# Kernel tuning notes

Measured on AMD Instinct MI355X. Metric: run time of the kernel, lower is better.

Reference implementation:

```python
import jax, jax.numpy as jnp
import numpy as np

L_MAX = 16          # static upper bound on ndimage label count (labels < 10 here)
SIGMA_AGG = 0.5
SIGMA_DIS = 3.0
ALPHA = 0.5
BETA = 0.25
EPS = 1e-6


def _seg(data, ids):
    return jax.ops.segment_sum(data, ids, num_segments=L_MAX)


def _safe_norm(sq):
    # sqrt with zero-safe gradient (matches torch.linalg.norm values)
    safe = jnp.where(sq > 0, sq, 1.0)
    return jnp.where(sq > 0, jnp.sqrt(safe), 0.0)


def _pan_loss(pred_regions, regions_gt, pred_kernels, kernels_gt,
              pred_similarities, lab_r4, lab_k4):
    B, C, H, W = pred_similarities.shape
    HW = H * W
    lab_k = lab_k4.reshape(B, HW)
    lab_r = lab_r4.reshape(B, HW)
    ker = kernels_gt.reshape(B, HW)
    sims = pred_similarities.reshape(B, C, HW)

    # ---- TextDiceLoss (ohem_masks = regions_gt, as in PANLoss.forward) ----
    ohem = regions_gt.reshape(B, -1)
    pr = jax.nn.sigmoid(pred_regions).reshape(B, -1) * ohem
    rg = regions_gt.reshape(B, -1) * ohem
    loss_regions = 1.0 - (2.0 * jnp.sum(pr * rg) + EPS) / (pr.sum() + rg.sum() + EPS)

    # ---- KernelDiceLoss ----
    pk = jax.nn.sigmoid(pred_kernels).reshape(B, -1)
    kg = kernels_gt.reshape(B, -1)
    loss_kernel = 1.0 - (2.0 * jnp.sum(pk * kg) + EPS) / (pk.sum() + kg.sum() + EPS)

    # ---- per-label segment sums (replaces the nested masked_select loops) ----
    seg_ker = jax.vmap(_seg)(ker, lab_k)  # [B,L] sum of kernels_mask per kernel label
    seg_sim = jax.vmap(lambda d, l: jax.vmap(lambda dc: _seg(dc, l))(d))(sims, lab_k)  # [B,C,L]
    # bug-faithful: region cardinality sums kernels_mask (not regions_mask) over region labels
    seg_reg = jax.vmap(_seg)(ker, lab_r)  # [B,L]

    pos_k = lab_k > 0
    card_k = jnp.where(pos_k, jnp.take_along_axis(seg_ker, lab_k, axis=1), 0.0)  # [B,HW]
    Gk = jnp.where(pos_k[:, None, :],
                   jnp.take_along_axis(seg_sim, lab_k[:, None, :], axis=2), 0.0)  # [B,C,HW]
    Gk = Gk / (card_k[:, None, :] + 1.0)
    card_r = jnp.where(lab_r > 0, jnp.take_along_axis(seg_reg, lab_r, axis=1), 0.0)  # [B,HW]

    # ---- AggregationLoss ----
    Fp = sims * regions_gt.reshape(B, 1, HW)
    sq = jnp.sum((Fp - Gk) ** 2, axis=1)          # [B,HW]
    nrm = _safe_norm(sq) - SIGMA_AGG
    nrm = jnp.where(nrm > 0.0, nrm, 0.0)
    D = jnp.log(nrm ** 2 + 1.0) / (card_r + 1.0)
    # bug-faithful: torch divides by num_kernel leaked from the LAST batch iteration
    num_k_last = lab_k[-1].max().astype(jnp.float32)
    L_agg = (D / num_k_last).sum()

    # ---- DiscriminationLoss (closed-form over the pairwise loop) ----
    # For pair (i,j) in batch b, ||Gi-Gj|| is ||S_i|| on label-i pixels (n_i of them),
    # ||S_j|| on label-j pixels, and 0 elsewhere (contributing f0=log(sigma^2+1)).
    K = lab_k.max(axis=1)                          # [B] kernels per image
    n = jax.vmap(_seg)(jnp.ones_like(ker), lab_k)  # [B,L] pixel counts per label
    sqS = jnp.sum(seg_sim ** 2, axis=1)            # [B,L]
    gap = SIGMA_DIS - _safe_norm(sqS)
    f = jnp.log(jnp.where(gap > 0.0, gap, 0.0) ** 2 + 1.0)  # [B,L]
    f0 = jnp.log(SIGMA_DIS ** 2 + 1.0)
    lvec = jnp.arange(L_MAX)
    valid = (lvec[None, :] >= 1) & (lvec[None, :] <= K[:, None])
    Kf = K.astype(jnp.float32)
    term1 = (Kf - 1.0) * jnp.sum(jnp.where(valid, n * (f - f0), 0.0), axis=1)
    term2 = Kf * (Kf - 1.0) / 2.0 * (B * HW) * f0
    L_dis = jnp.sum(jnp.where(K >= 2, term1 + term2, 0.0))

    return loss_regions + ALPHA * loss_kernel + BETA * (L_agg + L_dis)


def setup_inputs() -> dict:
    key = jax.random.key(0)
    ks = jax.random.split(key, 7)
    B, C, H, W = 8, 4, 896, 896
    return {
        "pred_regions": jax.random.normal(ks[0], (B, 1, H, W), jnp.float32),
        "regions_gt": jax.random.uniform(ks[1], (B, 1, H, W), jnp.float32),
        "pred_kernels": jax.random.normal(ks[2], (B, 1, H, W), jnp.float32),
        "kernels_gt": jax.random.uniform(ks[3], (B, 1, H, W), jnp.float32),
        "pred_similarities": jax.random.normal(ks[4], (B, C, H, W), jnp.float32),
        "text_mask_ndi_labels": jax.random.randint(ks[5], (B, 1, H, W), 0, 10, jnp.int32),
        "kernel_mask_ndi_labels": jax.random.randint(ks[6], (B, 1, H, W), 0, 10, jnp.int32),
    }


def reference(pred_regions, regions_gt, pred_kernels, kernels_gt,
              pred_similarities, text_mask_ndi_labels, kernel_mask_ndi_labels):
    return _pan_loss(pred_regions, regions_gt, pred_kernels, kernels_gt,
                     pred_similarities, text_mask_ndi_labels, kernel_mask_ndi_labels)
```

## Files before the change

kernel.cpp:

```cpp
#include <hip/hip_runtime.h>
#include <math.h>

#define NB 8
#define NC 4
#define HW 802816
#define LMAX 16
#define TPB 256
#define NWAVE (TPB/64)
#define VEC 4
#define IPTV 4
#define PXB (TPB*VEC*IPTV)
#define BPB (HW/PXB)
#define NSLOT 16

struct WS {
    float seg_ker[NSLOT][NB][LMAX];
    float seg_reg[NSLOT][NB][LMAX];
    float seg_n  [NSLOT][NB][LMAX];
    float seg_sim[NSLOT][NB][NC][LMAX];
    float dice   [NSLOT][6];
    int   kmax   [NSLOT][NB];
    float lagg;
};

__device__ __forceinline__ float waveReduceSum(float v) {
#pragma unroll
    for (int off = 32; off > 0; off >>= 1) v += __shfl_down(v, off, 64);
    return v;
}

#define REP9(M) M(1) M(2) M(3) M(4) M(5) M(6) M(7) M(8) M(9)

__global__ __launch_bounds__(TPB, 2) void pan1(
    const float* __restrict__ predR, const float* __restrict__ regGT,
    const float* __restrict__ predK, const float* __restrict__ kerGT,
    const float* __restrict__ sims,  const int* __restrict__ labR,
    const int* __restrict__ labK, WS* __restrict__ ws)
{
    const int b   = blockIdx.x / BPB;
    const int blk = blockIdx.x % BPB;
    const size_t pb = (size_t)b * HW;
    const int q0 = blk * PXB;
    const int lane = threadIdx.x & 63;
    const int wid  = threadIdx.x >> 6;

#define DECL_ACC(l) float aN##l=0.f, aK##l=0.f, aR##l=0.f, \
                          aS0_##l=0.f, aS1_##l=0.f, aS2_##l=0.f, aS3_##l=0.f;
    REP9(DECL_ACC)

    float d0=0.f,d1=0.f,d2=0.f,d3=0.f,d4=0.f,d5=0.f;
    int km = 0;

#pragma unroll
    for (int i = 0; i < IPTV; ++i) {
        const int q = q0 + ((i*TPB + threadIdx.x) << 2);
        const size_t p = pb + q;
        const float4 pr4 = *(const float4*)(predR + p);
        const float4 rg4 = *(const float4*)(regGT + p);
        const float4 pk4 = *(const float4*)(predK + p);
        const float4 kg4 = *(const float4*)(kerGT + p);
        const float4 sv0 = *(const float4*)(sims + ((size_t)(b*NC+0))*HW + q);
        const float4 sv1 = *(const float4*)(sims + ((size_t)(b*NC+1))*HW + q);
        const float4 sv2 = *(const float4*)(sims + ((size_t)(b*NC+2))*HW + q);
        const float4 sv3 = *(const float4*)(sims + ((size_t)(b*NC+3))*HW + q);
        const int4 lk4 = *(const int4*)(labK + p);
        const int4 lr4 = *(const int4*)(labR + p);

        const float prA[VEC] = {pr4.x, pr4.y, pr4.z, pr4.w};
        const float rgA[VEC] = {rg4.x, rg4.y, rg4.z, rg4.w};
        const float pkA[VEC] = {pk4.x, pk4.y, pk4.z, pk4.w};
        const float kgA[VEC] = {kg4.x, kg4.y, kg4.z, kg4.w};
        const float s0A[VEC] = {sv0.x, sv0.y, sv0.z, sv0.w};
        const float s1A[VEC] = {sv1.x, sv1.y, sv1.z, sv1.w};
        const float s2A[VEC] = {sv2.x, sv2.y, sv2.z, sv2.w};
        const float s3A[VEC] = {sv3.x, sv3.y, sv3.z, sv3.w};
        const int lkA[VEC] = {lk4.x, lk4.y, lk4.z, lk4.w};
        const int lrA[VEC] = {lr4.x, lr4.y, lr4.z, lr4.w};

#pragma unroll
        for (int j = 0; j < VEC; ++j) {
            const float rg = rgA[j], kg = kgA[j];
            const float sr = 1.f / (1.f + __expf(-prA[j]));
            const float sk = 1.f / (1.f + __expf(-pkA[j]));
            const float prm = sr * rg;
            const float rgm = rg * rg;
            d0 += prm * rgm; d1 += prm; d2 += rgm;
            d3 += sk * kg;   d4 += sk;  d5 += kg;

            const int lk = lkA[j];
            const int lr = lrA[j];
            km = max(km, lk);
            const float v0 = s0A[j], v1 = s1A[j], v2 = s2A[j], v3 = s3A[j];
#define UPD(l) { \
            const float fk = (lk == l) ? 1.f : 0.f; \
            const float fr = (lr == l) ? 1.f : 0.f; \
            aN##l += fk; \
            aK##l  = fmaf(fk, kg, aK##l); \
            aR##l  = fmaf(fr, kg, aR##l); \
            aS0_##l = fmaf(fk, v0, aS0_##l); \
            aS1_##l = fmaf(fk, v1, aS1_##l); \
            aS2_##l = fmaf(fk, v2, aS2_##l); \
            aS3_##l = fmaf(fk, v3, aS3_##l); }
            REP9(UPD)
#undef UPD
        }
    }

    __shared__ float s_part[NWAVE][72];
    __shared__ int   s_km[NWAVE];

#define WFLUSH(l) { \
    float r; \
    r = waveReduceSum(aN##l);   if (lane==0) s_part[wid][0*9 + (l-1)] = r; \
    r = waveReduceSum(aK##l);   if (lane==0) s_part[wid][1*9 + (l-1)] = r; \
    r = waveReduceSum(aR##l);   if (lane==0) s_part[wid][2*9 + (l-1)] = r; \
    r = waveReduceSum(aS0_##l); if (lane==0) s_part[wid][3*9 + (l-1)] = r; \
    r = waveReduceSum(aS1_##l); if (lane==0) s_part[wid][4*9 + (l-1)] = r; \
    r = waveReduceSum(aS2_##l); if (lane==0) s_part[wid][5*9 + (l-1)] = r; \
    r = waveReduceSum(aS3_##l); if (lane==0) s_part[wid][6*9 + (l-1)] = r; }
    REP9(WFLUSH)
#undef WFLUSH

    d0 = waveReduceSum(d0); d1 = waveReduceSum(d1); d2 = waveReduceSum(d2);
    d3 = waveReduceSum(d3); d4 = waveReduceSum(d4); d5 = waveReduceSum(d5);
#pragma unroll
    for (int off = 32; off > 0; off >>= 1) km = max(km, __shfl_down(km, off, 64));
    if (lane == 0) {
        s_part[wid][63]=d0; s_part[wid][64]=d1; s_part[wid][65]=d2;
        s_part[wid][66]=d3; s_part[wid][67]=d4; s_part[wid][68]=d5;
        s_km[wid] = km;
    }
    __syncthreads();

    const int slot = blockIdx.x & (NSLOT-1);
    if (threadIdx.x < 69) {
        const int t = threadIdx.x;
        const float s = s_part[0][t] + s_part[1][t] + s_part[2][t] + s_part[3][t];
        float* dst;
        if      (t <  9) dst = &ws->seg_n  [slot][b][t + 1];
        else if (t < 18) dst = &ws->seg_ker[slot][b][t - 8];
        else if (t < 27) dst = &ws->seg_reg[slot][b][t - 17];
        else if (t < 63) { const int u = t - 27; dst = &ws->seg_sim[slot][b][u/9][(u%9) + 1]; }
        else             dst = &ws->dice[slot][t - 63];
        unsafeAtomicAdd(dst, s);
    } else if (threadIdx.x == 69) {
        const int m = max(max(s_km[0], s_km[1]), max(s_km[2], s_km[3]));
        atomicMax(&ws->kmax[slot][b], m);
    }
}

__global__ __launch_bounds__(TPB) void pan_pass2(
    const float* __restrict__ regGT, const float* __restrict__ sims,
    const int* __restrict__ labR, const int* __restrict__ labK,
    WS* __restrict__ ws)
{
    const int b   = blockIdx.x / BPB;
    const int blk = blockIdx.x % BPB;
    const size_t pb = (size_t)b * HW;
    const int q0 = blk * PXB;

    __shared__ float s_ker[LMAX], s_reg[LMAX], s_sim[NC][LMAX];
    __shared__ float s_l[NWAVE];
    if (threadIdx.x < LMAX) {
        const int l = threadIdx.x;
        float k=0.f, r=0.f, c0=0.f, c1=0.f, c2=0.f, c3=0.f;
#pragma unroll
        for (int s = 0; s < NSLOT; ++s) {
            k  += ws->seg_ker[s][b][l];
            r  += ws->seg_reg[s][b][l];
            c0 += ws->seg_sim[s][b][0][l];
            c1 += ws->seg_sim[s][b][1][l];
            c2 += ws->seg_sim[s][b][2][l];
            c3 += ws->seg_sim[s][b][3][l];
        }
        s_ker[l]=k; s_reg[l]=r; s_sim[0][l]=c0; s_sim[1][l]=c1; s_sim[2][l]=c2; s_sim[3][l]=c3;
    }
    __syncthreads();

    float acc = 0.f;
#pragma unroll
    for (int i = 0; i < IPTV; ++i) {
        const int q = q0 + ((i*TPB + threadIdx.x) << 2);
        const size_t p = pb + q;
        const float4 rg4 = *(const float4*)(regGT + p);
        const float4 sv0 = *(const float4*)(sims + ((size_t)(b*NC+0))*HW + q);
        const float4 sv1 = *(const float4*)(sims + ((size_t)(b*NC+1))*HW + q);
        const float4 sv2 = *(const float4*)(sims + ((size_t)(b*NC+2))*HW + q);
        const float4 sv3 = *(const float4*)(sims + ((size_t)(b*NC+3))*HW + q);
        const int4 lk4 = *(const int4*)(labK + p);
        const int4 lr4 = *(const int4*)(labR + p);

        const float rgA[VEC] = {rg4.x, rg4.y, rg4.z, rg4.w};
        const float smA[NC][VEC] = {{sv0.x,sv0.y,sv0.z,sv0.w},{sv1.x,sv1.y,sv1.z,sv1.w},
                                    {sv2.x,sv2.y,sv2.z,sv2.w},{sv3.x,sv3.y,sv3.z,sv3.w}};
        const int lkA[VEC] = {lk4.x, lk4.y, lk4.z, lk4.w};
        const int lrA[VEC] = {lr4.x, lr4.y, lr4.z, lr4.w};

#pragma unroll
        for (int j = 0; j < VEC; ++j) {
            const int lk = lkA[j] & (LMAX-1);
            const int lr = lrA[j] & (LMAX-1);
            const float rg = rgA[j];
            const float ck = (lk > 0) ? s_ker[lk] : 0.f;
            const float cr = (lr > 0) ? s_reg[lr] : 0.f;
            const float inv = 1.f / (ck + 1.f);
            float sq = 0.f;
#pragma unroll
            for (int c = 0; c < NC; ++c) {
                const float Fp = smA[c][j] * rg;
                const float G  = (lk > 0) ? s_sim[c][lk] * inv : 0.f;
                const float d  = Fp - G;
                sq += d * d;
            }
            float nr = (sq > 0.f) ? sqrtf(sq) : 0.f;
            nr -= 0.5f;
            nr  = fmaxf(nr, 0.f);
            acc += __logf(nr*nr + 1.f) / (cr + 1.f);
        }
    }
    acc = waveReduceSum(acc);
    const int wid = threadIdx.x >> 6;
    if ((threadIdx.x & 63) == 0) s_l[wid] = acc;
    __syncthreads();
    if (threadIdx.x == 0) {
        float s = 0.f;
#pragma unroll
        for (int w = 0; w < NWAVE; ++w) s += s_l[w];
        unsafeAtomicAdd(&ws->lagg, s);
    }
}

__global__ void pan_finalize(const WS* __restrict__ ws, float* __restrict__ out)
{
    if (threadIdx.x != 0 || blockIdx.x != 0) return;
    const double f0 = log(10.0);
    double Ldis = 0.0;
    int kmaxb[NB];
    for (int b = 0; b < NB; ++b) {
        int m = 0;
        for (int s = 0; s < NSLOT; ++s) m = max(m, ws->kmax[s][b]);
        kmaxb[b] = m;
    }
    for (int b = 0; b < NB; ++b) {
        const int K = kmaxb[b];
        if (K >= 2) {
            double t1 = 0.0;
            const int lim = (K < LMAX-1) ? K : (LMAX-1);
            for (int l = 1; l <= lim; ++l) {
                float sqS = 0.f;
                for (int c = 0; c < NC; ++c) {
                    float S = 0.f;
                    for (int s = 0; s < NSLOT; ++s) S += ws->seg_sim[s][b][c][l];
                    sqS += S * S;
                }
                float n_l = 0.f;
                for (int s = 0; s < NSLOT; ++s) n_l += ws->seg_n[s][b][l];
                const float nm  = (sqS > 0.f) ? sqrtf(sqS) : 0.f;
                float gap = 3.0f - nm;
                gap = fmaxf(gap, 0.f);
                const double f = log((double)gap*gap + 1.0);
                t1 += (double)n_l * (f - f0);
            }
            Ldis += (K - 1.0) * t1
                  + (double)K * (K - 1) * 0.5 * (double)NB * (double)HW * f0;
        }
    }
    double dice[6];
    for (int j = 0; j < 6; ++j) {
        double s = 0.0;
        for (int sl = 0; sl < NSLOT; ++sl) s += ws->dice[sl][j];
        dice[j] = s;
    }
    const double numk = (double)kmaxb[NB-1];
    const double Lagg = (double)ws->lagg / numk;
    const double lr = 1.0 - (2.0*dice[0] + 1e-6) / (dice[1] + dice[2] + 1e-6);
    const double lk = 1.0 - (2.0*dice[3] + 1e-6) / (dice[4] + dice[5] + 1e-6);
    out[0] = (float)(lr + 0.5*lk + 0.25*(Lagg + Ldis));
}

extern "C" void kernel_launch(void* const* d_in, const int* in_sizes, int n_in,
                              void* d_out, int out_size, void* d_ws, size_t ws_size,
                              hipStream_t stream)
{
    const float* predR = (const float*)d_in[0];
    const float* regGT = (const float*)d_in[1];
    const float* predK = (const float*)d_in[2];
    const float* kerGT = (const float*)d_in[3];
    const float* sims  = (const float*)d_in[4];
    const int*   labR  = (const int*)d_in[5];
    const int*   labK  = (const int*)d_in[6];
    WS* ws = (WS*)d_ws;

    hipMemsetAsync(d_ws, 0, sizeof(WS), stream);

    pan1     <<<dim3(NB * BPB), dim3(TPB), 0, stream>>>(predR, regGT, predK, kerGT, sims, labR, labK, ws);
    pan_pass2<<<dim3(NB * BPB), dim3(TPB), 0, stream>>>(regGT, sims, labR, labK, ws);
    pan_finalize<<<1, 64, 0, stream>>>(ws, (float*)d_out);
}
```

Before: 209.2 us.

## Move dice sums into second pass and slim segment-sum kernel

The dice reductions (sigmoid over predR/predK) move out of the first segment-sum pass into the aggregation pass, so the first kernel only reads kerGT, sims and the labels and runs with a tighter launch bound. Per-label pixel counts now come from ballot/popcount as integers, and the max label is inferred from the nonzero counts, which drops a float accumulator and a shuffle-max reduction. The second pass now reads predR, predK and kerGT in addition to its previous inputs, so total memory traffic stays about the same but is spread differently across the two kernels. The aim is lower register pressure and higher occupancy in the heavy first kernel.

```diff
diff --git a/kernel.cpp b/kernel.cpp
--- a/kernel.cpp
+++ b/kernel.cpp
@@ -31,7 +31,104 @@
 
 #define REP9(M) M(1) M(2) M(3) M(4) M(5) M(6) M(7) M(8) M(9)
 
-__global__ __launch_bounds__(TPB, 2) void pan1(
+__global__ __launch_bounds__(TPB, 4) void pan_segs(
+    const float* __restrict__ kerGT, const float* __restrict__ sims,
+    const int* __restrict__ labK, const int* __restrict__ labR,
+    WS* __restrict__ ws)
+{
+    const int b   = blockIdx.x / BPB;
+    const int blk = blockIdx.x % BPB;
+    const size_t pb = (size_t)b * HW;
+    const int q0 = blk * PXB;
+    const int lane = threadIdx.x & 63;
+    const int wid  = threadIdx.x >> 6;
+
+#define DECL_ACC(l) float aK##l=0.f, aR##l=0.f, \
+                          aS0_##l=0.f, aS1_##l=0.f, aS2_##l=0.f, aS3_##l=0.f; \
+                    int cN##l = 0;
+    REP9(DECL_ACC)
+#undef DECL_ACC
+
+#pragma unroll
+    for (int i = 0; i < IPTV; ++i) {
+        const int q = q0 + ((i*TPB + threadIdx.x) << 2);
+        const size_t p = pb + q;
+        const float4 kg4 = *(const float4*)(kerGT + p);
+        const float4 sv0 = *(const float4*)(sims + ((size_t)(b*NC+0))*HW + q);
+        const float4 sv1 = *(const float4*)(sims + ((size_t)(b*NC+1))*HW + q);
+        const float4 sv2 = *(const float4*)(sims + ((size_t)(b*NC+2))*HW + q);
+        const float4 sv3 = *(const float4*)(sims + ((size_t)(b*NC+3))*HW + q);
+        const int4 lk4 = *(const int4*)(labK + p);
+        const int4 lr4 = *(const int4*)(labR + p);
+
+        const float kgA[VEC] = {kg4.x, kg4.y, kg4.z, kg4.w};
+        const float s0A[VEC] = {sv0.x, sv0.y, sv0.z, sv0.w};
+        const float s1A[VEC] = {sv1.x, sv1.y, sv1.z, sv1.w};
+        const float s2A[VEC] = {sv2.x, sv2.y, sv2.z, sv2.w};
+        const float s3A[VEC] = {sv3.x, sv3.y, sv3.z, sv3.w};
+        const int lkA[VEC] = {lk4.x, lk4.y, lk4.z, lk4.w};
+        const int lrA[VEC] = {lr4.x, lr4.y, lr4.z, lr4.w};
+
+#pragma unroll
+        for (int j = 0; j < VEC; ++j) {
+            const float kg = kgA[j];
+            const int lk = lkA[j];
+            const int lr = lrA[j];
+            const float v0 = s0A[j], v1 = s1A[j], v2 = s2A[j], v3 = s3A[j];
+#define UPDK(l) { \
+            cN##l += (int)__popcll(__ballot(lk == l)); \
+            const float fk = (lk == l) ? 1.f : 0.f; \
+            aK##l  = fmaf(fk, kg, aK##l); \
+            aS0_##l = fmaf(fk, v0, aS0_##l); \
+            aS1_##l = fmaf(fk, v1, aS1_##l); \
+            aS2_##l = fmaf(fk, v2, aS2_##l); \
+            aS3_##l = fmaf(fk, v3, aS3_##l); \
+            const float fr = (lr == l) ? 1.f : 0.f; \
+            aR##l  = fmaf(fr, kg, aR##l); }
+            REP9(UPDK)
+#undef UPDK
+        }
+    }
+
+    __shared__ float s_part[NWAVE][63];
+    __shared__ int   s_km[NWAVE];
+
+#define WFLUSH(l) { \
+    float r; \
+    r = waveReduceSum(aK##l);   if (lane==0) s_part[wid][ 0 + (l-1)] = r; \
+    r = waveReduceSum(aR##l);   if (lane==0) s_part[wid][ 9 + (l-1)] = r; \
+    r = waveReduceSum(aS0_##l); if (lane==0) s_part[wid][18 + (l-1)] = r; \
+    r = waveReduceSum(aS1_##l); if (lane==0) s_part[wid][27 + (l-1)] = r; \
+    r = waveReduceSum(aS2_##l); if (lane==0) s_part[wid][36 + (l-1)] = r; \
+    r = waveReduceSum(aS3_##l); if (lane==0) s_part[wid][45 + (l-1)] = r; \
+    if (lane==0) s_part[wid][54 + (l-1)] = (float)cN##l; }
+    REP9(WFLUSH)
+#undef WFLUSH
+
+    int km = 0;
+#define KMCHK(l) if (cN##l) km = l;
+    REP9(KMCHK)
+#undef KMCHK
+    if (lane == 0) s_km[wid] = km;
+    __syncthreads();
+
+    const int slot = blockIdx.x & (NSLOT-1);
+    if (threadIdx.x < 63) {
+        const int t = threadIdx.x;
+        const float s = s_part[0][t] + s_part[1][t] + s_part[2][t] + s_part[3][t];
+        float* dst;
+        if      (t <  9) dst = &ws->seg_ker[slot][b][t + 1];
+        else if (t < 18) dst = &ws->seg_reg[slot][b][t - 9 + 1];
+        else if (t < 54) { const int u = t - 18; dst = &ws->seg_sim[slot][b][u/9][(u%9) + 1]; }
+        else             dst = &ws->seg_n[slot][b][t - 54 + 1];
+        unsafeAtomicAdd(dst, s);
+    } else if (threadIdx.x == 63) {
+        const int m = max(max(s_km[0], s_km[1]), max(s_km[2], s_km[3]));
+        atomicMax(&ws->kmax[slot][b], m);
+    }
+}
+
+__global__ __launch_bounds__(TPB) void pan_pass2(
     const float* __restrict__ predR, const float* __restrict__ regGT,
     const float* __restrict__ predK, const float* __restrict__ kerGT,
     const float* __restrict__ sims,  const int* __restrict__ labR,
@@ -44,13 +141,26 @@
     const int lane = threadIdx.x & 63;
     const int wid  = threadIdx.x >> 6;
 
-#define DECL_ACC(l) float aN##l=0.f, aK##l=0.f, aR##l=0.f, \
-                          aS0_##l=0.f, aS1_##l=0.f, aS2_##l=0.f, aS3_##l=0.f;
-    REP9(DECL_ACC)
+    __shared__ float s_ker[LMAX], s_reg[LMAX], s_sim[NC][LMAX];
+    __shared__ float s_part[NWAVE][7];
+    if (threadIdx.x < LMAX) {
+        const int l = threadIdx.x;
+        float k=0.f, r=0.f, c0=0.f, c1=0.f, c2=0.f, c3=0.f;
+#pragma unroll
+        for (int s = 0; s < NSLOT; ++s) {
+            k  += ws->seg_ker[s][b][l];
+            r  += ws->seg_reg[s][b][l];
+            c0 += ws->seg_sim[s][b][0][l];
+            c1 += ws->seg_sim[s][b][1][l];
+            c2 += ws->seg_sim[s][b][2][l];
+            c3 += ws->seg_sim[s][b][3][l];
+        }
+        s_ker[l]=k; s_reg[l]=r; s_sim[0][l]=c0; s_sim[1][l]=c1; s_sim[2][l]=c2; s_sim[3][l]=c3;
+    }
+    __syncthreads();
 
     float d0=0.f,d1=0.f,d2=0.f,d3=0.f,d4=0.f,d5=0.f;
-    int km = 0;
-
+    float acc = 0.f;
 #pragma unroll
     for (int i = 0; i < IPTV; ++i) {
         const int q = q0 + ((i*TPB + threadIdx.x) << 2);
@@ -70,10 +180,8 @@
         const float rgA[VEC] = {rg4.x, rg4.y, rg4.z, rg4.w};
         const float pkA[VEC] = {pk4.x, pk4.y, pk4.z, pk4.w};
         const float kgA[VEC] = {kg4.x, kg4.y, kg4.z, kg4.w};
-        const float s0A[VEC] = {sv0.x, sv0.y, sv0.z, sv0.w};
-        const float s1A[VEC] = {sv1.x, sv1.y, sv1.z, sv1.w};
-        const float s2A[VEC] = {sv2.x, sv2.y, sv2.z, sv2.w};
-        const float s3A[VEC] = {sv3.x, sv3.y, sv3.z, sv3.w};
+        const float smA[NC][VEC] = {{sv0.x,sv0.y,sv0.z,sv0.w},{sv1.x,sv1.y,sv1.z,sv1.w},
+                                    {sv2.x,sv2.y,sv2.z,sv2.w},{sv3.x,sv3.y,sv3.z,sv3.w}};
         const int lkA[VEC] = {lk4.x, lk4.y, lk4.z, lk4.w};
         const int lrA[VEC] = {lr4.x, lr4.y, lr4.z, lr4.w};
 
@@ -87,120 +195,8 @@
             d0 += prm * rgm; d1 += prm; d2 += rgm;
             d3 += sk * kg;   d4 += sk;  d5 += kg;
 
-            const int lk = lkA[j];
-            const int lr = lrA[j];
-            km = max(km, lk);
-            const float v0 = s0A[j], v1 = s1A[j], v2 = s2A[j], v3 = s3A[j];
-#define UPD(l) { \
-            const float fk = (lk == l) ? 1.f : 0.f; \
-            const float fr = (lr == l) ? 1.f : 0.f; \
-            aN##l += fk; \
-            aK##l  = fmaf(fk, kg, aK##l); \
-            aR##l  = fmaf(fr, kg, aR##l); \
-            aS0_##l = fmaf(fk, v0, aS0_##l); \
-            aS1_##l = fmaf(fk, v1, aS1_##l); \
-            aS2_##l = fmaf(fk, v2, aS2_##l); \
-            aS3_##l = fmaf(fk, v3, aS3_##l); }
-            REP9(UPD)
-#undef UPD
-        }
-    }
-
-    __shared__ float s_part[NWAVE][72];
-    __shared__ int   s_km[NWAVE];
-
-#define WFLUSH(l) { \
-    float r; \
-    r = waveReduceSum(aN##l);   if (lane==0) s_part[wid][0*9 + (l-1)] = r; \
-    r = waveReduceSum(aK##l);   if (lane==0) s_part[wid][1*9 + (l-1)] = r; \
-    r = waveReduceSum(aR##l);   if (lane==0) s_part[wid][2*9 + (l-1)] = r; \
-    r = waveReduceSum(aS0_##l); if (lane==0) s_part[wid][3*9 + (l-1)] = r; \
-    r = waveReduceSum(aS1_##l); if (lane==0) s_part[wid][4*9 + (l-1)] = r; \
-    r = waveReduceSum(aS2_##l); if (lane==0) s_part[wid][5*9 + (l-1)] = r; \
-    r = waveReduceSum(aS3_##l); if (lane==0) s_part[wid][6*9 + (l-1)] = r; }
-    REP9(WFLUSH)
-#undef WFLUSH
-
-    d0 = waveReduceSum(d0); d1 = waveReduceSum(d1); d2 = waveReduceSum(d2);
-    d3 = waveReduceSum(d3); d4 = waveReduceSum(d4); d5 = waveReduceSum(d5);
-#pragma unroll
-    for (int off = 32; off > 0; off >>= 1) km = max(km, __shfl_down(km, off, 64));
-    if (lane == 0) {
-        s_part[wid][63]=d0; s_part[wid][64]=d1; s_part[wid][65]=d2;
-        s_part[wid][66]=d3; s_part[wid][67]=d4; s_part[wid][68]=d5;
-        s_km[wid] = km;
-    }
-    __syncthreads();
-
-    const int slot = blockIdx.x & (NSLOT-1);
-    if (threadIdx.x < 69) {
-        const int t = threadIdx.x;
-        const float s = s_part[0][t] + s_part[1][t] + s_part[2][t] + s_part[3][t];
-        float* dst;
-        if      (t <  9) dst = &ws->seg_n  [slot][b][t + 1];
-        else if (t < 18) dst = &ws->seg_ker[slot][b][t - 8];
-        else if (t < 27) dst = &ws->seg_reg[slot][b][t - 17];
-        else if (t < 63) { const int u = t - 27; dst = &ws->seg_sim[slot][b][u/9][(u%9) + 1]; }
-        else             dst = &ws->dice[slot][t - 63];
-        unsafeAtomicAdd(dst, s);
-    } else if (threadIdx.x == 69) {
-        const int m = max(max(s_km[0], s_km[1]), max(s_km[2], s_km[3]));
-        atomicMax(&ws->kmax[slot][b], m);
-    }
-}
-
-__global__ __launch_bounds__(TPB) void pan_pass2(
-    const float* __restrict__ regGT, const float* __restrict__ sims,
-    const int* __restrict__ labR, const int* __restrict__ labK,
-    WS* __restrict__ ws)
-{
-    const int b   = blockIdx.x / BPB;
-    const int blk = blockIdx.x % BPB;
-    const size_t pb = (size_t)b * HW;
-    const int q0 = blk * PXB;
-
-    __shared__ float s_ker[LMAX], s_reg[LMAX], s_sim[NC][LMAX];
-    __shared__ float s_l[NWAVE];
-    if (threadIdx.x < LMAX) {
-        const int l = threadIdx.x;
-        float k=0.f, r=0.f, c0=0.f, c1=0.f, c2=0.f, c3=0.f;
-#pragma unroll
-        for (int s = 0; s < NSLOT; ++s) {
-            k  += ws->seg_ker[s][b][l];
-            r  += ws->seg_reg[s][b][l];
-            c0 += ws->seg_sim[s][b][0][l];
-            c1 += ws->seg_sim[s][b][1][l];
-            c2 += ws->seg_sim[s][b][2][l];
-            c3 += ws->seg_sim[s][b][3][l];
-        }
-        s_ker[l]=k; s_reg[l]=r; s_sim[0][l]=c0; s_sim[1][l]=c1; s_sim[2][l]=c2; s_sim[3][l]=c3;
-    }
-    __syncthreads();
-
-    float acc = 0.f;
-#pragma unroll
-    for (int i = 0; i < IPTV; ++i) {
-        const int q = q0 + ((i*TPB + threadIdx.x) << 2);
-        const size_t p = pb + q;
-        const float4 rg4 = *(const float4*)(regGT + p);
-        const float4 sv0 = *(const float4*)(sims + ((size_t)(b*NC+0))*HW + q);
-        const float4 sv1 = *(const float4*)(sims + ((size_t)(b*NC+1))*HW + q);
-        const float4 sv2 = *(const float4*)(sims + ((size_t)(b*NC+2))*HW + q);
-        const float4 sv3 = *(const float4*)(sims + ((size_t)(b*NC+3))*HW + q);
-        const int4 lk4 = *(const int4*)(labK + p);
-        const int4 lr4 = *(const int4*)(labR + p);
-
-        const float rgA[VEC] = {rg4.x, rg4.y, rg4.z, rg4.w};
-        const float smA[NC][VEC] = {{sv0.x,sv0.y,sv0.z,sv0.w},{sv1.x,sv1.y,sv1.z,sv1.w},
-                                    {sv2.x,sv2.y,sv2.z,sv2.w},{sv3.x,sv3.y,sv3.z,sv3.w}};
-        const int lkA[VEC] = {lk4.x, lk4.y, lk4.z, lk4.w};
-        const int lrA[VEC] = {lr4.x, lr4.y, lr4.z, lr4.w};
-
-#pragma unroll
-        for (int j = 0; j < VEC; ++j) {
             const int lk = lkA[j] & (LMAX-1);
             const int lr = lrA[j] & (LMAX-1);
-            const float rg = rgA[j];
             const float ck = (lk > 0) ? s_ker[lk] : 0.f;
             const float cr = (lr > 0) ? s_reg[lr] : 0.f;
             const float inv = 1.f / (ck + 1.f);
@@ -218,15 +214,22 @@
             acc += __logf(nr*nr + 1.f) / (cr + 1.f);
         }
     }
+
+    d0 = waveReduceSum(d0); d1 = waveReduceSum(d1); d2 = waveReduceSum(d2);
+    d3 = waveReduceSum(d3); d4 = waveReduceSum(d4); d5 = waveReduceSum(d5);
     acc = waveReduceSum(acc);
-    const int wid = threadIdx.x >> 6;
-    if ((threadIdx.x & 63) == 0) s_l[wid] = acc;
+    if (lane == 0) {
+        s_part[wid][0]=d0; s_part[wid][1]=d1; s_part[wid][2]=d2;
+        s_part[wid][3]=d3; s_part[wid][4]=d4; s_part[wid][5]=d5;
+        s_part[wid][6]=acc;
+    }
     __syncthreads();
-    if (threadIdx.x == 0) {
-        float s = 0.f;
-#pragma unroll
-        for (int w = 0; w < NWAVE; ++w) s += s_l[w];
-        unsafeAtomicAdd(&ws->lagg, s);
+    const int slot = blockIdx.x & (NSLOT-1);
+    if (threadIdx.x < 7) {
+        const int t = threadIdx.x;
+        const float s = s_part[0][t] + s_part[1][t] + s_part[2][t] + s_part[3][t];
+        if (t < 6) unsafeAtomicAdd(&ws->dice[slot][t], s);
+        else       unsafeAtomicAdd(&ws->lagg, s);
     }
 }
 
@@ -293,7 +296,7 @@
 
     hipMemsetAsync(d_ws, 0, sizeof(WS), stream);
 
-    pan1     <<<dim3(NB * BPB), dim3(TPB), 0, stream>>>(predR, regGT, predK, kerGT, sims, labR, labK, ws);
-    pan_pass2<<<dim3(NB * BPB), dim3(TPB), 0, stream>>>(regGT, sims, labR, labK, ws);
+    pan_segs <<<dim3(NB * BPB), dim3(TPB), 0, stream>>>(kerGT, sims, labK, labR, ws);
+    pan_pass2<<<dim3(NB * BPB), dim3(TPB), 0, stream>>>(predR, regGT, predK, kerGT, sims, labR, labK, ws);
     pan_finalize<<<1, 64, 0, stream>>>(ws, (float*)d_out);
 }
```

Result: faster. 180.6 us (-13.6%).
